# Optimization experiments

Measured on AMD Instinct MI355X. Metric: run time of the kernel, lower is better.

The kernel has to match this reference:

```python
import jax, jax.numpy as jnp
import numpy as np

WS = 7      # window size
SHIFT = 3   # shift size
NH = 6      # num heads
C = 192     # channels
HH = 56
WW = 56
B = 32


def _rel_coords():
    ch, cw = np.meshgrid(np.arange(WS), np.arange(WS), indexing='ij')
    coords = np.stack([ch, cw]).reshape(2, -1)            # (2, 49)
    rel = coords[:, :, None] - coords[:, None, :]          # (2, 49, 49)
    rel[0] += WS - 1
    rel[1] += WS - 1
    rel[0] *= 2 * WS - 1
    return rel.sum(0)                                      # (49, 49)


def _swin_attn_mask(Hp, Wp):
    img = np.zeros((Hp, Wp), np.int32)
    cnt = 0
    for hs in (slice(0, -WS), slice(-WS, -SHIFT), slice(-SHIFT, None)):
        for ws_ in (slice(0, -WS), slice(-WS, -SHIFT), slice(-SHIFT, None)):
            img[hs, ws_] = cnt
            cnt += 1
    win = img.reshape(Hp // WS, WS, Wp // WS, WS).transpose(0, 2, 1, 3).reshape(-1, WS * WS)
    return win[:, :, None] != win[:, None, :]              # (Nw, 49, 49) bool


def setup_inputs() -> dict:
    key = jax.random.key(0)
    ks = jax.random.split(key, 8)
    s = 0.02
    return {
        'x': jax.random.normal(ks[0], (B, HH * WW, C), jnp.float32),
        'H': HH,
        'W': WW,
        'attn_mask': jnp.asarray(_swin_attn_mask(HH, WW)),
        'relative_coords': jnp.asarray(_rel_coords(), jnp.int32),
        'norm1_w': jnp.ones((C,), jnp.float32),
        'norm1_b': jnp.zeros((C,), jnp.float32),
        'qkv_w': jax.random.normal(ks[1], (3 * C, C), jnp.float32) * s,
        'rel_bias': jax.random.normal(ks[2], ((2 * WS - 1) ** 2, NH), jnp.float32) * 0.2,
        'proj_w': jax.random.normal(ks[3], (C, C), jnp.float32) * s,
        'proj_b': jnp.zeros((C,), jnp.float32),
        'norm2_w': jnp.ones((C,), jnp.float32),
        'norm2_b': jnp.zeros((C,), jnp.float32),
        'fc1_w': jax.random.normal(ks[4], (4 * C, C), jnp.float32) * s,
        'fc1_b': jnp.zeros((4 * C,), jnp.float32),
        'fc2_w': jax.random.normal(ks[5], (C, 4 * C), jnp.float32) * s,
        'fc2_b': jnp.zeros((C,), jnp.float32),
    }


def _ln(t, w, b):
    m = t.mean(-1, keepdims=True)
    v = t.var(-1, keepdims=True)
    return (t - m) / jnp.sqrt(v + 1e-5) * w + b


def reference(x, H, W, attn_mask, relative_coords, norm1_w, norm1_b, qkv_w, rel_bias,
              proj_w, proj_b, norm2_w, norm2_b, fc1_w, fc1_b, fc2_w, fc2_b):
    Bb, L, Cd = x.shape
    nh, hd = NH, C // NH
    shortcut = x
    h = _ln(x, norm1_w, norm1_b).reshape(Bb, H, W, Cd)
    pad_h = (WS - H % WS) % WS
    pad_w = (WS - W % WS) % WS
    if pad_h or pad_w:
        h = jnp.pad(h, ((0, 0), (0, pad_h), (0, pad_w), (0, 0)))
    Hp, Wp = H + pad_h, W + pad_w
    if SHIFT > 0:
        h = jnp.roll(h, (-SHIFT, -SHIFT), axis=(1, 2))
    nWh, nWw = Hp // WS, Wp // WS
    Lw = WS * WS
    win = h.reshape(Bb, nWh, WS, nWw, WS, Cd).transpose(0, 1, 3, 2, 4, 5).reshape(-1, Lw, Cd)
    B_ = win.shape[0]
    qkv = (win @ qkv_w.T).reshape(B_, Lw, 3, nh, hd).transpose(2, 0, 3, 1, 4)
    q, k, v = qkv[0], qkv[1], qkv[2]
    # NOTE: source multiplies by num_dim**0.5 (faithful quirk)
    attn = jnp.einsum('bhid,bhjd->bhij', q, k) * (Cd ** 0.5)
    bias = rel_bias[relative_coords].transpose(2, 0, 1)    # (nh, Lw, Lw)
    attn = attn + bias[None]
    if SHIFT > 0:
        Nw = attn_mask.shape[0]
        attn = attn.reshape(-1, Nw, nh, Lw, Lw)
        attn = jnp.where(attn_mask[None, :, None], -100.0, attn)
        attn = attn.reshape(B_, nh, Lw, Lw)
    attn = jax.nn.softmax(attn, axis=-1)
    out = jnp.einsum('bhij,bhjd->bhid', attn, v).transpose(0, 2, 1, 3).reshape(B_, Lw, Cd)
    out = out @ proj_w.T + proj_b
    out = out.reshape(Bb, nWh, nWw, WS, WS, Cd).transpose(0, 1, 3, 2, 4, 5).reshape(Bb, Hp, Wp, Cd)
    if SHIFT > 0:
        out = jnp.roll(out, (SHIFT, SHIFT), axis=(1, 2))
    out = out[:, :H, :W].reshape(Bb, L, Cd)
    x = shortcut + out
    h2 = _ln(x, norm2_w, norm2_b)
    h2 = jax.nn.gelu(h2 @ fc1_w.T + fc1_b, approximate=False)
    # source MLP applies GELU (drop2 = act_layer()) after fc2 (faithful quirk)
    h2 = jax.nn.gelu(h2 @ fc2_w.T + fc2_b, approximate=False)
    return x + h2
```

## Files before the change

### kernel.cpp

```cpp
#include <hip/hip_runtime.h>

#define WS7    7
#define SHIFT3 3
#define NHEAD  6
#define CCH    192
#define HDIM   32
#define HH56   56
#define LTOK   (HH56*HH56)
#define NWIN   64
#define NBATCH 32
#define NWTOT  (NBATCH*NWIN)
#define LW     49
#define MTOK   (NWTOT*LW)

typedef unsigned short u16;
typedef unsigned int   u32;
typedef __bf16 b16;
typedef b16   b16x8 __attribute__((ext_vector_type(8)));
typedef u16   u16x8 __attribute__((ext_vector_type(8)));
typedef float f32x4 __attribute__((ext_vector_type(4)));

__device__ __forceinline__ float b2f(u16 u) {
    u32 x = ((u32)u) << 16;
    return __builtin_bit_cast(float, x);
}
__device__ __forceinline__ u16 f2b(float f) {
    u32 x = __builtin_bit_cast(u32, f);
    u32 r = x + 0x7FFFu + ((x >> 16) & 1u);
    return (u16)(r >> 16);
}
__device__ __forceinline__ float gelu_exact(float x) {
    return 0.5f * x * (1.0f + erff(x * 0.7071067811865475f));
}

__device__ __forceinline__ int map_token(int m, int &b) {
    int widx = m / LW, p = m - widx * LW;
    b = widx >> 6;
    int wloc = widx & 63;
    int wh = wloc >> 3, ww = wloc & 7;
    int i = p / WS7, j = p - i * WS7;
    int gh = wh * WS7 + i + SHIFT3; if (gh >= HH56) gh -= HH56;
    int gw = ww * WS7 + j + SHIFT3; if (gw >= HH56) gw -= HH56;
    return gh * HH56 + gw;
}

__global__ __launch_bounds__(1024) void probe_kernel(const u16* __restrict__ x, int* flag) {
    __shared__ int ch, cz;
    if (threadIdx.x == 0) { ch = 0; cz = 0; }
    __syncthreads();
    int i = threadIdx.x * 16;
    u16x8 a = *(const u16x8*)(x + i);
    u16x8 b = *(const u16x8*)(x + i + 8);
    int h = 0, z = 0;
    #pragma unroll
    for (int q = 0; q < 8; q++) {
        h += (((a[q] >> 7) & 0xFF) >= 0xC0) + (((b[q] >> 7) & 0xFF) >= 0xC0);
        z += (a[q] == 0) + (b[q] == 0);
    }
    #pragma unroll
    for (int off = 32; off > 0; off >>= 1) {
        h += __shfl_xor(h, off, 64);
        z += __shfl_xor(z, off, 64);
    }
    if ((threadIdx.x & 63) == 0) { atomicAdd(&ch, h); atomicAdd(&cz, z); }
    __syncthreads();
    if (threadIdx.x == 0) *flag = (ch > 250 || cz > 2048) ? 1 : 0;
}

#define CANON_TOTAL 445302
__global__ __launch_bounds__(256) void canon_all_kernel(
    const int* __restrict__ flag,
    const void* s0, const void* s1, const void* s2,  const void* s3,
    const void* s4, const void* s5, const void* s6,  const void* s7,
    const void* s8, const void* s9, const void* s10, const void* s11,
    char* __restrict__ ws)
{
    int i = blockIdx.x * 256 + threadIdx.x;
    if (i >= CANON_TOTAL) return;
    const void* srcs[12] = {s0, s1, s2, s3, s4, s5, s6, s7, s8, s9, s10, s11};
    const int cnt[12] = {110592, 36864, 147456, 147456, 192, 192, 192, 192, 192, 768, 192, 1014};
    const int off[12] = {64, 221248, 294976, 589888, 884800, 885184, 885568, 885952, 886336, 886720, 888256, 888640};
    int seg = 0, base = 0;
    while (seg < 11 && i >= base + cnt[seg]) { base += cnt[seg]; seg++; }
    int j = i - base;
    const void* sp = srcs[seg];
    u16* dp = (u16*)(ws + off[seg]);
    dp[j] = (*flag) ? f2b(((const float*)sp)[j]) : ((const u16*)sp)[j];
}

template<int GATHER>
__global__ __launch_bounds__(256) void ln_kernel(
    const void* __restrict__ src, const u16* __restrict__ w, const u16* __restrict__ bia,
    u16* __restrict__ dst, int m_base, const int* __restrict__ flag)
{
    int wave = threadIdx.x >> 6, lane = threadIdx.x & 63;
    int mloc = blockIdx.x * 4 + wave;
    size_t row;
    if (GATHER) { int b; int l = map_token(m_base + mloc, b); row = (size_t)b * LTOK + l; }
    else row = mloc;
    float v0, v1, v2;
    if (GATHER && *flag) {
        const float* xp = (const float*)src + row * CCH;
        v0 = xp[lane]; v1 = xp[lane + 64]; v2 = xp[lane + 128];
    } else {
        const u16* xp = (const u16*)src + row * CCH;
        v0 = b2f(xp[lane]); v1 = b2f(xp[lane + 64]); v2 = b2f(xp[lane + 128]);
    }
    float s = v0 + v1 + v2, sq = v0 * v0 + v1 * v1 + v2 * v2;
    for (int off = 32; off > 0; off >>= 1) {
        s  += __shfl_xor(s, off, 64);
        sq += __shfl_xor(sq, off, 64);
    }
    float mean = s * (1.f / 192.f);
    float var  = fmaxf(sq * (1.f / 192.f) - mean * mean, 0.f);
    float rstd = rsqrtf(var + 1e-5f);
    u16* op = dst + (size_t)mloc * CCH;
    op[lane]       = f2b((v0 - mean) * rstd * b2f(w[lane])       + b2f(bia[lane]));
    op[lane + 64]  = f2b((v1 - mean) * rstd * b2f(w[lane + 64])  + b2f(bia[lane + 64]));
    op[lane + 128] = f2b((v2 - mean) * rstd * b2f(w[lane + 128]) + b2f(bia[lane + 128]));
}

template<int ROWS>
__device__ __forceinline__ void stageT(const u16* __restrict__ g, int ldk, u16* s, int tid) {
    constexpr int CH = ROWS * 5;
    constexpr int ITER = (CH + 255) / 256;
    #pragma unroll
    for (int it = 0; it < ITER; it++) {
        int t = it * 256 + tid;
        if ((CH % 256 == 0) || t < CH) {
            int row = t / 5, c = t - row * 5;
            int cc = (c == 4) ? 0 : c;
            const u16* src = g + (size_t)row * ldk + cc * 8;
            u16* dst = s + (size_t)(it * 256 + (tid & ~63)) * 8;
            __builtin_amdgcn_global_load_lds(
                (const __attribute__((address_space(1))) void*)src,
                (__attribute__((address_space(3))) void*)dst, 16, 0, 0);
        }
    }
}

template<int MODE, int KK>
__global__ __launch_bounds__(256, 3) void gemm_t(
    const u16* __restrict__ A, const u16* __restrict__ Bm,
    const u16* __restrict__ bias,
    u16* __restrict__ Cb, u16* __restrict__ X1, const void* __restrict__ Xin,
    void* __restrict__ Oout, size_t o_off, int m_base,
    const int* __restrict__ flag)
{
    __shared__ __align__(16) u16 As[2][128 * 40];
    __shared__ __align__(16) u16 Bs[2][192 * 40];
    int tid = threadIdx.x;
    int m0 = blockIdx.x * 128, n0 = blockIdx.y * 192;
    int wave = tid >> 6, lane = tid & 63;
    int wm = wave >> 1, wn = wave & 1;
    int quad = lane >> 4, mr = lane & 15;

    const u16* Ag = A + (size_t)m0 * KK;
    const u16* Bg = Bm + (size_t)n0 * KK;

    stageT<128>(Ag, KK, As[0], tid);
    stageT<192>(Bg, KK, Bs[0], tid);
    __syncthreads();

    f32x4 acc[4][6] = {};
    constexpr int NSTEP = KK / 32;

    #pragma unroll 1
    for (int t = 0; t < NSTEP; t++) {
        int cur = t & 1;
        if (t + 1 < NSTEP) {
            stageT<128>(Ag + (t + 1) * 32, KK, As[cur ^ 1], tid);
            stageT<192>(Bg + (t + 1) * 32, KK, Bs[cur ^ 1], tid);
        }
        const u16* pa = &As[cur][(wm * 64 + mr) * 40 + quad * 8];
        const u16* pb = &Bs[cur][(wn * 96 + mr) * 40 + quad * 8];
        b16x8 a[4], b[6];
        #pragma unroll
        for (int sm = 0; sm < 4; sm++)
            a[sm] = __builtin_bit_cast(b16x8, *(const u16x8*)(pa + sm * 16 * 40));
        #pragma unroll
        for (int sn = 0; sn < 6; sn++)
            b[sn] = __builtin_bit_cast(b16x8, *(const u16x8*)(pb + sn * 16 * 40));
        #pragma unroll
        for (int sm = 0; sm < 4; sm++)
            #pragma unroll
            for (int sn = 0; sn < 6; sn++)
                acc[sm][sn] = __builtin_amdgcn_mfma_f32_16x16x32_bf16(a[sm], b[sn], acc[sm][sn], 0, 0, 0);
        __syncthreads();
    }

    int isf = *flag;
    #pragma unroll
    for (int sm = 0; sm < 4; sm++) {
        #pragma unroll
        for (int r = 0; r < 4; r++) {
            int mm = m0 + wm * 64 + sm * 16 + quad * 4 + r;
            int bimg = 0, limg = 0;
            if (MODE == 1) { limg = map_token(m_base + mm, bimg); }
            #pragma unroll
            for (int sn = 0; sn < 6; sn++) {
                float val = acc[sm][sn][r];
                int nn = n0 + wn * 96 + sn * 16 + mr;
                if (MODE == 0) {
                    Cb[(size_t)mm * 576 + nn] = f2b(val);
                } else if (MODE == 1) {
                    val += b2f(bias[nn]);
                    size_t idx = ((size_t)bimg * LTOK + limg) * CCH + nn;
                    float xi = isf ? ((const float*)Xin)[idx] : b2f(((const u16*)Xin)[idx]);
                    X1[idx] = f2b(xi + val);
                } else if (MODE == 2) {
                    val = gelu_exact(val + b2f(bias[nn]));
                    Cb[(size_t)mm * 768 + nn] = f2b(val);
                } else {
                    val = gelu_exact(val + b2f(bias[nn]));
                    size_t idx = (size_t)mm * CCH + nn;
                    float r2 = val + b2f(X1[idx]);
                    if (isf) ((float*)Oout)[o_off + idx] = r2;
                    else     ((u16*)Oout)[o_off + idx]  = f2b(r2);
                }
            }
        }
    }
}

__global__ __launch_bounds__(256) void attn_kernel(
    const u16* __restrict__ qkv, const u16* __restrict__ rel_bias,
    u16* __restrict__ aout)
{
    __shared__ __align__(16) u16 qs[64 * 32];
    __shared__ __align__(16) u16 ks[64 * 32];
    __shared__ __align__(16) u16 vsT[32 * 72];
    __shared__ __align__(16) u16 ps[64 * 72];
    __shared__ float bias_s[169];
    int blk = blockIdx.x;
    int widx = blk / NHEAD, head = blk - widx * NHEAD;
    int wloc = widx & 63;
    int wh = wloc >> 3, ww = wloc & 7;
    int tid = threadIdx.x;
    const u16* base = qkv + (size_t)widx * LW * 576 + head * HDIM;

    if (tid < 196) {
        int i = tid >> 2, c8 = (tid & 3) * 8;
        *(uint4*)&qs[i * 32 + c8] = *(const uint4*)(base + (size_t)i * 576 + c8);
        *(uint4*)&ks[i * 32 + c8] = *(const uint4*)(base + (size_t)i * 576 + 192 + c8);
        u16x8 vv = *(const u16x8*)(base + (size_t)i * 576 + 384 + c8);
        #pragma unroll
        for (int q = 0; q < 8; q++) vsT[(c8 + q) * 72 + i] = vv[q];
    }
    for (int idx = tid; idx < 32 * 15; idx += 256) {
        int d = idx / 15, j = 49 + (idx - d * 15);
        vsT[d * 72 + j] = 0;
    }
    if (tid < 169) bias_s[tid] = b2f(rel_bias[tid * NHEAD + head]);
    __syncthreads();

    int wave = tid >> 6, lane = tid & 63;
    int quad = lane >> 4, c = lane & 15;

    b16x8 aq = __builtin_bit_cast(b16x8, *(const u16x8*)&qs[(wave * 16 + c) * 32 + quad * 8]);
    f32x4 sacc[4];
    #pragma unroll
    for (int nt = 0; nt < 4; nt++) {
        b16x8 bk = __builtin_bit_cast(b16x8, *(const u16x8*)&ks[(nt * 16 + c) * 32 + quad * 8]);
        f32x4 z = {};
        sacc[nt] = __builtin_amdgcn_mfma_f32_16x16x32_bf16(aq, bk, z, 0, 0, 0);
    }

    const float SCALE = 13.856406460551018f;
    float val[4][4];
    int rbase = wave * 16 + quad * 4;
    #pragma unroll
    for (int r = 0; r < 4; r++) {
        int i = rbase + r;
        int ih = i / WS7, iw = i - ih * WS7;
        int ri = (wh == 7 ? (ih < 4 ? 1 : 2) : 0) * 3 + (ww == 7 ? (iw < 4 ? 1 : 2) : 0);
        #pragma unroll
        for (int nt = 0; nt < 4; nt++) {
            int j = nt * 16 + c;
            float v;
            if (i >= LW) v = 0.f;
            else if (j >= LW) v = -1e30f;
            else {
                int jh = j / WS7, jw = j - jh * WS7;
                int rj = (wh == 7 ? (jh < 4 ? 1 : 2) : 0) * 3 + (ww == 7 ? (jw < 4 ? 1 : 2) : 0);
                if (ri != rj) v = -100.0f;
                else v = fmaf(sacc[nt][r], SCALE, bias_s[(ih - jh + 6) * 13 + (iw - jw + 6)]);
            }
            val[r][nt] = v;
        }
    }

    #pragma unroll
    for (int r = 0; r < 4; r++) {
        float mx = fmaxf(fmaxf(val[r][0], val[r][1]), fmaxf(val[r][2], val[r][3]));
        for (int d = 1; d < 16; d <<= 1) mx = fmaxf(mx, __shfl_xor(mx, d, 64));
        float sum = 0.f;
        #pragma unroll
        for (int nt = 0; nt < 4; nt++) { float e = expf(val[r][nt] - mx); val[r][nt] = e; sum += e; }
        for (int d = 1; d < 16; d <<= 1) sum += __shfl_xor(sum, d, 64);
        float inv = 1.f / sum;
        int i = rbase + r;
        #pragma unroll
        for (int nt = 0; nt < 4; nt++)
            ps[i * 72 + nt * 16 + c] = f2b(val[r][nt] * inv);
    }

    f32x4 oacc[2] = {{}, {}};
    #pragma unroll
    for (int kh = 0; kh < 2; kh++) {
        b16x8 ap = __builtin_bit_cast(b16x8, *(const u16x8*)&ps[(wave * 16 + c) * 72 + kh * 32 + quad * 8]);
        #pragma unroll
        for (int nt = 0; nt < 2; nt++) {
            b16x8 bv = __builtin_bit_cast(b16x8, *(const u16x8*)&vsT[(nt * 16 + c) * 72 + kh * 32 + quad * 8]);
            oacc[nt] = __builtin_amdgcn_mfma_f32_16x16x32_bf16(ap, bv, oacc[nt], 0, 0, 0);
        }
    }
    #pragma unroll
    for (int nt = 0; nt < 2; nt++) {
        #pragma unroll
        for (int r = 0; r < 4; r++) {
            int i = rbase + r;
            if (i < LW)
                aout[((size_t)widx * LW + i) * CCH + head * HDIM + nt * 16 + c] = f2b(oacc[nt][r]);
        }
    }
}

extern "C" void kernel_launch(void* const* d_in, const int* in_sizes, int n_in,
                              void* d_out, int out_size, void* d_ws, size_t ws_size,
                              hipStream_t stream)
{
    const void* x_in = d_in[0];
    char* ws = (char*)d_ws;
    int* flag = (int*)ws;

    u16* qkvw_c  = (u16*)(ws + 64);
    u16* projw_c = (u16*)(ws + 221248);
    u16* fc1w_c  = (u16*)(ws + 294976);
    u16* fc2w_c  = (u16*)(ws + 589888);
    u16* n1w_c   = (u16*)(ws + 884800);
    u16* n1b_c   = (u16*)(ws + 885184);
    u16* n2w_c   = (u16*)(ws + 885568);
    u16* n2b_c   = (u16*)(ws + 885952);
    u16* projb_c = (u16*)(ws + 886336);
    u16* fc1b_c  = (u16*)(ws + 886720);
    u16* fc2b_c  = (u16*)(ws + 888256);
    u16* relb_c  = (u16*)(ws + 888640);

    const size_t P0 = 1u << 20;
    const size_t X1SZ   = (size_t)MTOK * CCH * 2;
    const size_t QKVSZ  = (size_t)MTOK * 576 * 2;

    u16* x1 = (u16*)(ws + P0);

    probe_kernel<<<1, 1024, 0, stream>>>((const u16*)x_in, flag);
    canon_all_kernel<<<(CANON_TOTAL + 255) / 256, 256, 0, stream>>>(
        flag,
        d_in[7], d_in[9], d_in[13], d_in[15],
        d_in[5], d_in[6], d_in[11], d_in[12],
        d_in[10], d_in[14], d_in[16], d_in[8],
        ws);

    if (ws_size >= P0 + 3 * X1SZ + QKVSZ) {
        u16* winq = (u16*)(ws + P0 + X1SZ);
        u16* aout = (u16*)(ws + P0 + 2 * X1SZ);
        u16* qkvq = (u16*)(ws + P0 + 3 * X1SZ);
        u16* h1q  = aout;

        ln_kernel<1><<<MTOK / 4, 256, 0, stream>>>(x_in, n1w_c, n1b_c, winq, 0, flag);
        gemm_t<0, 192><<<dim3(MTOK / 128, 3), 256, 0, stream>>>(
            winq, qkvw_c, nullptr, qkvq, nullptr, nullptr, nullptr, 0, 0, flag);
        attn_kernel<<<NWTOT * NHEAD, 256, 0, stream>>>(qkvq, relb_c, aout);
        gemm_t<1, 192><<<dim3(MTOK / 128, 1), 256, 0, stream>>>(
            aout, projw_c, projb_c, nullptr, x1, x_in, nullptr, 0, 0, flag);
        ln_kernel<0><<<MTOK / 4, 256, 0, stream>>>(x1, n2w_c, n2b_c, winq, 0, flag);
        gemm_t<2, 192><<<dim3(MTOK / 128, 4), 256, 0, stream>>>(
            winq, fc1w_c, fc1b_c, h1q, nullptr, nullptr, nullptr, 0, 0, flag);
        gemm_t<3, 768><<<dim3(MTOK / 128, 1), 256, 0, stream>>>(
            h1q, fc2w_c, fc2b_c, nullptr, x1, nullptr, d_out, 0, 0, flag);
    } else {
        const int QC = 8, EC = 8;
        const int MQ = MTOK / QC, ME = MTOK / EC;
        u16* winq = (u16*)(ws + P0 + X1SZ);
        u16* aout = (u16*)(ws + P0 + X1SZ + (size_t)MQ * CCH * 2);
        u16* qkvq = (u16*)(ws + P0 + X1SZ + 2 * (size_t)MQ * CCH * 2);
        u16* h1q  = winq;

        for (int q = 0; q < QC; q++) {
            int mb = q * MQ;
            ln_kernel<1><<<MQ / 4, 256, 0, stream>>>(x_in, n1w_c, n1b_c, winq, mb, flag);
            gemm_t<0, 192><<<dim3(MQ / 128, 3), 256, 0, stream>>>(
                winq, qkvw_c, nullptr, qkvq, nullptr, nullptr, nullptr, 0, mb, flag);
            attn_kernel<<<(NWTOT / QC) * NHEAD, 256, 0, stream>>>(qkvq, relb_c, aout);
            gemm_t<1, 192><<<dim3(MQ / 128, 1), 256, 0, stream>>>(
                aout, projw_c, projb_c, nullptr, x1, x_in, nullptr, 0, mb, flag);
        }
        u16* xnq = (u16*)(ws + P0 + X1SZ + (size_t)ME * 768 * 2);
        for (int e = 0; e < EC; e++) {
            size_t off = (size_t)e * ME * CCH;
            ln_kernel<0><<<ME / 4, 256, 0, stream>>>(x1 + off, n2w_c, n2b_c, xnq, 0, flag);
            gemm_t<2, 192><<<dim3(ME / 128, 4), 256, 0, stream>>>(
                xnq, fc1w_c, fc1b_c, h1q, nullptr, nullptr, nullptr, 0, 0, flag);
            gemm_t<3, 768><<<dim3(ME / 128, 1), 256, 0, stream>>>(
                h1q, fc2w_c, fc2b_c, nullptr, x1 + off, nullptr, d_out, off, 0, flag);
        }
    }
}
```

Baseline: 619.2 us.

## Swizzle GEMM LDS tiles and use explicit vmcnt waits for async staging

Replaces the padded 40-element LDS row layout, which issued a redundant fifth load per row, with a dense 32-element row layout. An XOR swizzle on the 16-byte chunk index avoids bank conflicts, and the staging loop drops its bounds check. The double-buffered loop now waits with s_waitcnt vmcnt(5) so the next tile's global-to-LDS loads stay in flight while the current tile is consumed, framed by raw s_barrier and sched_barrier in place of __syncthreads. This cuts LDS footprint and load count and improves overlap. The risk is that the hand-tuned vmcnt count and barriers must match the exact number of loads issued per stage.

```diff
diff --git a/kernel.cpp b/kernel.cpp
--- a/kernel.cpp
+++ b/kernel.cpp
@@ -121,21 +121,18 @@
 }
 
 template<int ROWS>
-__device__ __forceinline__ void stageT(const u16* __restrict__ g, int ldk, u16* s, int tid) {
-    constexpr int CH = ROWS * 5;
-    constexpr int ITER = (CH + 255) / 256;
+__device__ __forceinline__ void stageL(const u16* __restrict__ g, int ldk, u16* s, int tid) {
+    constexpr int ITER = ROWS * 4 / 256;
     #pragma unroll
     for (int it = 0; it < ITER; it++) {
         int t = it * 256 + tid;
-        if ((CH % 256 == 0) || t < CH) {
-            int row = t / 5, c = t - row * 5;
-            int cc = (c == 4) ? 0 : c;
-            const u16* src = g + (size_t)row * ldk + cc * 8;
-            u16* dst = s + (size_t)(it * 256 + (tid & ~63)) * 8;
-            __builtin_amdgcn_global_load_lds(
-                (const __attribute__((address_space(1))) void*)src,
-                (__attribute__((address_space(3))) void*)dst, 16, 0, 0);
-        }
+        int row = t >> 2, c = t & 3;
+        int cc = c ^ ((row >> 1) & 3);
+        const u16* src = g + (size_t)row * ldk + cc * 8;
+        u16* dst = s + (size_t)(it * 256 + (tid & ~63)) * 8;
+        __builtin_amdgcn_global_load_lds(
+            (const __attribute__((address_space(1))) void*)src,
+            (__attribute__((address_space(3))) void*)dst, 16, 0, 0);
     }
 }
 
@@ -147,8 +144,8 @@
     void* __restrict__ Oout, size_t o_off, int m_base,
     const int* __restrict__ flag)
 {
-    __shared__ __align__(16) u16 As[2][128 * 40];
-    __shared__ __align__(16) u16 Bs[2][192 * 40];
+    __shared__ __align__(16) u16 As[2][128 * 32];
+    __shared__ __align__(16) u16 Bs[2][192 * 32];
     int tid = threadIdx.x;
     int m0 = blockIdx.x * 128, n0 = blockIdx.y * 192;
     int wave = tid >> 6, lane = tid & 63;
@@ -158,9 +155,8 @@
     const u16* Ag = A + (size_t)m0 * KK;
     const u16* Bg = Bm + (size_t)n0 * KK;
 
-    stageT<128>(Ag, KK, As[0], tid);
-    stageT<192>(Bg, KK, Bs[0], tid);
-    __syncthreads();
+    stageL<128>(Ag, KK, As[0], tid);
+    stageL<192>(Bg, KK, Bs[0], tid);
 
     f32x4 acc[4][6] = {};
     constexpr int NSTEP = KK / 32;
@@ -169,24 +165,34 @@
     for (int t = 0; t < NSTEP; t++) {
         int cur = t & 1;
         if (t + 1 < NSTEP) {
-            stageT<128>(Ag + (t + 1) * 32, KK, As[cur ^ 1], tid);
-            stageT<192>(Bg + (t + 1) * 32, KK, Bs[cur ^ 1], tid);
-        }
-        const u16* pa = &As[cur][(wm * 64 + mr) * 40 + quad * 8];
-        const u16* pb = &Bs[cur][(wn * 96 + mr) * 40 + quad * 8];
+            stageL<128>(Ag + (t + 1) * 32, KK, As[cur ^ 1], tid);
+            stageL<192>(Bg + (t + 1) * 32, KK, Bs[cur ^ 1], tid);
+            asm volatile("s_waitcnt vmcnt(5)");
+        } else {
+            asm volatile("s_waitcnt vmcnt(0)");
+        }
+        __builtin_amdgcn_s_barrier();
+        __builtin_amdgcn_sched_barrier(0);
         b16x8 a[4], b[6];
         #pragma unroll
-        for (int sm = 0; sm < 4; sm++)
-            a[sm] = __builtin_bit_cast(b16x8, *(const u16x8*)(pa + sm * 16 * 40));
-        #pragma unroll
-        for (int sn = 0; sn < 6; sn++)
-            b[sn] = __builtin_bit_cast(b16x8, *(const u16x8*)(pb + sn * 16 * 40));
+        for (int sm = 0; sm < 4; sm++) {
+            int row = wm * 64 + sm * 16 + mr;
+            a[sm] = __builtin_bit_cast(b16x8,
+                *(const u16x8*)&As[cur][row * 32 + (quad ^ ((row >> 1) & 3)) * 8]);
+        }
+        #pragma unroll
+        for (int sn = 0; sn < 6; sn++) {
+            int row = wn * 96 + sn * 16 + mr;
+            b[sn] = __builtin_bit_cast(b16x8,
+                *(const u16x8*)&Bs[cur][row * 32 + (quad ^ ((row >> 1) & 3)) * 8]);
+        }
         #pragma unroll
         for (int sm = 0; sm < 4; sm++)
             #pragma unroll
             for (int sn = 0; sn < 6; sn++)
                 acc[sm][sn] = __builtin_amdgcn_mfma_f32_16x16x32_bf16(a[sm], b[sn], acc[sm][sn], 0, 0, 0);
-        __syncthreads();
+        __builtin_amdgcn_sched_barrier(0);
+        __builtin_amdgcn_s_barrier();
     }
 
     int isf = *flag;
```

After: 606.9 us. 2.0% less time.
